# Kernel tuning notes

Hardware: AMD Instinct MI355X
Metric: run time of the kernel (lower is better)

## Reference

```python
import jax, jax.numpy as jnp
import numpy as np

N = 16777216

def setup_inputs() -> dict:
    key = jax.random.key(0)
    k1, k2 = jax.random.split(key)
    pred = jax.random.uniform(k1, (N, 2), dtype=jnp.float32)
    target = jax.random.randint(k2, (N,), 0, 2, dtype=jnp.int64)
    return {"pred": pred, "target": target}

def reference(pred, target):
    p0 = pred[:, 0]
    p1 = pred[:, 1]
    is_zero = target == 0
    # per-element squared error depending on class
    sq = jnp.where(is_zero,
                   (1.0 - p0) ** 2 + p1 ** 2,
                   p0 ** 2 + (1.0 - p1) ** 2)
    # +2 penalty when the wrong logit is larger
    wrong = jnp.where(is_zero, p0 < p1, p1 < p0)
    penalty = jnp.where(wrong, jnp.float32(2.0), jnp.float32(0.0))
    loss = jnp.sum(sq + penalty) / pred.shape[0]
    return loss
```

## Files before the change

### kernel.cpp

```cpp
#include <hip/hip_runtime.h>

#define BLOCK 256
#define GRID 2048

__global__ __launch_bounds__(BLOCK) void loss_partial_kernel(
    const float* __restrict__ pred,
    const int* __restrict__ target,
    float* __restrict__ partials,
    int n4)
{
    const float4* __restrict__ pred4 = reinterpret_cast<const float4*>(pred);
    const int4* __restrict__ tgt4 = reinterpret_cast<const int4*>(target);

    float acc = 0.0f;
    const int stride = gridDim.x * blockDim.x;
    for (int i = blockIdx.x * blockDim.x + threadIdx.x; i < n4; i += stride) {
        float4 pa = pred4[2 * i];
        float4 pb = pred4[2 * i + 1];
        int4 t = tgt4[i];

        float p0[4] = {pa.x, pa.z, pb.x, pb.z};
        float p1[4] = {pa.y, pa.w, pb.y, pb.w};
        int tt[4] = {t.x, t.y, t.z, t.w};

#pragma unroll
        for (int k = 0; k < 4; ++k) {
            bool z = (tt[k] == 0);
            float a = z ? p0[k] : p1[k];
            float b = z ? p1[k] : p0[k];
            float d = 1.0f - a;
            float s = fmaf(d, d, b * b);
            s += (a < b) ? 2.0f : 0.0f;
            acc += s;
        }
    }

#pragma unroll
    for (int off = 32; off > 0; off >>= 1)
        acc += __shfl_down(acc, off, 64);

    __shared__ float wsum[BLOCK / 64];
    const int lane = threadIdx.x & 63;
    const int wid = threadIdx.x >> 6;
    if (lane == 0) wsum[wid] = acc;
    __syncthreads();
    if (threadIdx.x == 0) {
        float s = 0.0f;
#pragma unroll
        for (int w = 0; w < BLOCK / 64; ++w) s += wsum[w];
        partials[blockIdx.x] = s;
    }
}

__global__ __launch_bounds__(BLOCK) void loss_final_kernel(
    const float* __restrict__ partials, float* __restrict__ out,
    int nparts, float inv_n)
{
    float acc = 0.0f;
    for (int i = threadIdx.x; i < nparts; i += BLOCK)
        acc += partials[i];

#pragma unroll
    for (int off = 32; off > 0; off >>= 1)
        acc += __shfl_down(acc, off, 64);

    __shared__ float wsum[BLOCK / 64];
    const int lane = threadIdx.x & 63;
    const int wid = threadIdx.x >> 6;
    if (lane == 0) wsum[wid] = acc;
    __syncthreads();
    if (threadIdx.x == 0) {
        float s = 0.0f;
#pragma unroll
        for (int w = 0; w < BLOCK / 64; ++w) s += wsum[w];
        out[0] = s * inv_n;
    }
}

extern "C" void kernel_launch(void* const* d_in, const int* in_sizes, int n_in,
                              void* d_out, int out_size, void* d_ws, size_t ws_size,
                              hipStream_t stream) {
    const float* pred = (const float*)d_in[0];
    const int* target = (const int*)d_in[1];
    float* out = (float*)d_out;
    float* partials = (float*)d_ws;

    int n = in_sizes[1];
    if (n * 2 != in_sizes[0]) n = in_sizes[0] / 2;
    const int n4 = n / 4;

    loss_partial_kernel<<<GRID, BLOCK, 0, stream>>>(pred, target, partials, n4);
    loss_final_kernel<<<1, BLOCK, 0, stream>>>(partials, out, GRID, 1.0f / (float)n);
}
```

Before: 232.8 us.

## Use per-block contiguous chunks with unrolled batched loads of pred and target

Replaces the grid-stride loop with a contiguous range of element pairs per block. Each thread issues four independent float4/int2 loads before computing, which raises the number of memory requests in flight. Elements are now processed in pairs (one float4 of predictions with one int2 of targets) instead of groups of four, and a remainder loop handles the tail. The intent is better bandwidth through more loads in flight and more regular streaming per block, at the cost of smaller individual target loads.

Measured after the change: 235.0 us. Within noise of the previous version (+0.9%).

```diff
diff --git a/kernel.cpp b/kernel.cpp
--- a/kernel.cpp
+++ b/kernel.cpp
@@ -2,36 +2,64 @@
 
 #define BLOCK 256
 #define GRID 2048
+#define UNROLL 4
 
 __global__ __launch_bounds__(BLOCK) void loss_partial_kernel(
-    const float* __restrict__ pred,
-    const int* __restrict__ target,
+    const float4* __restrict__ pred4,
+    const int2*  __restrict__ tgt2,
     float* __restrict__ partials,
-    int n4)
+    int npairs)
 {
-    const float4* __restrict__ pred4 = reinterpret_cast<const float4*>(pred);
-    const int4* __restrict__ tgt4 = reinterpret_cast<const int4*>(target);
+    const int ppb  = (npairs + GRID - 1) / GRID;
+    const int base = blockIdx.x * ppb;
+    const int end  = min(base + ppb, npairs);
 
     float acc = 0.0f;
-    const int stride = gridDim.x * blockDim.x;
-    for (int i = blockIdx.x * blockDim.x + threadIdx.x; i < n4; i += stride) {
-        float4 pa = pred4[2 * i];
-        float4 pb = pred4[2 * i + 1];
-        int4 t = tgt4[i];
+    int k = base + threadIdx.x;
 
-        float p0[4] = {pa.x, pa.z, pb.x, pb.z};
-        float p1[4] = {pa.y, pa.w, pb.y, pb.w};
-        int tt[4] = {t.x, t.y, t.z, t.w};
-
+    for (; k + (UNROLL - 1) * BLOCK < end; k += UNROLL * BLOCK) {
+        float4 p[UNROLL];
+        int2   t[UNROLL];
 #pragma unroll
-        for (int k = 0; k < 4; ++k) {
-            bool z = (tt[k] == 0);
-            float a = z ? p0[k] : p1[k];
-            float b = z ? p1[k] : p0[k];
+        for (int u = 0; u < UNROLL; ++u) p[u] = pred4[k + u * BLOCK];
+#pragma unroll
+        for (int u = 0; u < UNROLL; ++u) t[u] = tgt2[k + u * BLOCK];
+#pragma unroll
+        for (int u = 0; u < UNROLL; ++u) {
+            {
+                bool z = (t[u].x == 0);
+                float a = z ? p[u].x : p[u].y;
+                float b = z ? p[u].y : p[u].x;
+                float d = 1.0f - a;
+                float s = fmaf(d, d, b * b);
+                acc += s + ((a < b) ? 2.0f : 0.0f);
+            }
+            {
+                bool z = (t[u].y == 0);
+                float a = z ? p[u].z : p[u].w;
+                float b = z ? p[u].w : p[u].z;
+                float d = 1.0f - a;
+                float s = fmaf(d, d, b * b);
+                acc += s + ((a < b) ? 2.0f : 0.0f);
+            }
+        }
+    }
+    for (; k < end; k += BLOCK) {
+        float4 p = pred4[k];
+        int2   t = tgt2[k];
+        {
+            bool z = (t.x == 0);
+            float a = z ? p.x : p.y;
+            float b = z ? p.y : p.x;
             float d = 1.0f - a;
-            float s = fmaf(d, d, b * b);
-            s += (a < b) ? 2.0f : 0.0f;
-            acc += s;
+            acc += fmaf(d, d, b * b) + ((a < b) ? 2.0f : 0.0f);
+        }
+        {
+            bool z = (t.y == 0);
+            float a = z ? p.z : p.w;
+            float b = z ? p.w : p.z;
+            float d = 1.0f - a;
+            acc += fmaf(d, d, b * b) + ((a < b) ? 2.0f : 0.0f);
         }
     }
 
@@ -41,7 +69,7 @@
 
     __shared__ float wsum[BLOCK / 64];
     const int lane = threadIdx.x & 63;
-    const int wid = threadIdx.x >> 6;
+    const int wid  = threadIdx.x >> 6;
     if (lane == 0) wsum[wid] = acc;
     __syncthreads();
     if (threadIdx.x == 0) {
@@ -66,7 +94,7 @@
 
     __shared__ float wsum[BLOCK / 64];
     const int lane = threadIdx.x & 63;
-    const int wid = threadIdx.x >> 6;
+    const int wid  = threadIdx.x >> 6;
     if (lane == 0) wsum[wid] = acc;
     __syncthreads();
     if (threadIdx.x == 0) {
@@ -87,8 +115,9 @@
 
     int n = in_sizes[1];
     if (n * 2 != in_sizes[0]) n = in_sizes[0] / 2;
-    const int n4 = n / 4;
+    const int npairs = n / 2;
 
-    loss_partial_kernel<<<GRID, BLOCK, 0, stream>>>(pred, target, partials, n4);
+    loss_partial_kernel<<<GRID, BLOCK, 0, stream>>>(
+        (const float4*)pred, (const int2*)target, partials, npairs);
     loss_final_kernel<<<1, BLOCK, 0, stream>>>(partials, out, GRID, 1.0f / (float)n);
 }
```
